# Kernel optimization log

Measured on AMD Instinct MI355X. Metric: run time of the kernel, lower is better.

## Reference

```python
import jax, jax.numpy as jnp
import numpy as np

N_NODES = 50000
N_EDGES = 800000


def setup_inputs() -> dict:
    key = jax.random.key(0)
    ks = jax.random.split(key, 12)
    x = jax.random.normal(ks[0], (N_NODES, 500), dtype=jnp.float32)
    edge_src = jax.random.randint(ks[1], (N_EDGES,), 0, N_NODES, dtype=jnp.int32)
    edge_dst = jax.random.randint(ks[2], (N_EDGES,), 0, N_NODES, dtype=jnp.int32)
    edge_vals = jax.random.uniform(ks[3], (N_EDGES,), dtype=jnp.float32) * 0.1
    def w(k, fan_in, fan_out):
        s = 1.0 / np.sqrt(fan_in)
        return jax.random.uniform(k, (fan_in, fan_out), dtype=jnp.float32, minval=-s, maxval=s)
    W1 = w(ks[4], 500, 128)
    b1 = jnp.zeros((128,), jnp.float32)
    W2 = w(ks[5], 128, 64)
    b2 = jnp.zeros((64,), jnp.float32)
    W3 = w(ks[6], 64, 16)
    b3 = jnp.zeros((16,), jnp.float32)
    We = w(ks[7], 64, 64)
    be = jnp.zeros((64,), jnp.float32)
    return {"x": x, "edge_vals": edge_vals, "W1": W1, "b1": b1, "W2": W2,
            "b2": b2, "W3": W3, "b3": b3, "We": We, "be": be,
            "edge_src": edge_src, "edge_dst": edge_dst}


def reference(x, edge_vals, W1, b1, W2, b2, W3, b3, We, be, edge_src, edge_dst):
    n = x.shape[0]

    def gcn_layer(h, W, b):
        # GraphConvolution: support = h @ W ; out = spmm(adj, support) + b
        support = h @ W                                   # [N, d_out]
        msg = support[edge_dst] * edge_vals[:, None]      # [E, d_out]
        agg = jax.ops.segment_sum(msg, edge_src, num_segments=n)
        return agg + b

    h = jax.nn.relu(gcn_layer(x, W1, b1))
    # dropout omitted (eval mode, training=False)
    h = jax.nn.relu(gcn_layer(h, W2, b2))
    out1 = jax.nn.log_softmax(gcn_layer(h, W3, b3), axis=1)
    out2 = h @ We + be
    return (out1, out2)
```

## Files before the change

kernel.cpp:

```cpp
#include <hip/hip_runtime.h>
#include <math.h>

#define N_NODES 50000
#define N_EDGES 800000

typedef __attribute__((ext_vector_type(8))) short bf16x8;
typedef __attribute__((ext_vector_type(4))) float f32x4;

__device__ inline unsigned short f2bf(float f) {
    unsigned u = __float_as_uint(f);
    unsigned r = (u + 0x7fffu + ((u >> 16) & 1u)) >> 16;
    return (unsigned short)r;
}

__global__ __launch_bounds__(256) void convert_weights_kernel(
    const float* __restrict__ W1, const float* __restrict__ W2,
    const float* __restrict__ We, const float* __restrict__ W3,
    unsigned short* __restrict__ W1bf, unsigned short* __restrict__ W2bf,
    unsigned short* __restrict__ Wcat)
{
    int t = blockIdx.x * 256 + threadIdx.x;
    if (t < 65536) {
        int n = t >> 9, k = t & 511;
        float v = (k < 500) ? W1[k * 128 + n] : 0.0f;
        W1bf[t] = f2bf(v);
    } else if (t < 65536 + 8192) {
        int t2 = t - 65536;
        int n = t2 >> 7, k = t2 & 127;
        W2bf[t2] = f2bf(W2[k * 64 + n]);
    } else if (t < 65536 + 8192 + 5120) {
        int t3 = t - 65536 - 8192;
        int n = t3 >> 6, k = t3 & 63;
        float v = (n < 64) ? We[k * 64 + n] : W3[k * 16 + (n - 64)];
        Wcat[t3] = f2bf(v);
    }
}

__global__ __launch_bounds__(256) void gemm1_mfma_kernel(
    const float* __restrict__ A,
    const unsigned short* __restrict__ Bt,
    unsigned short* __restrict__ C)
{
    const int wid  = (blockIdx.x * 256 + threadIdx.x) >> 6;
    const int lane = threadIdx.x & 63;
    const int r = lane & 15, q = lane >> 4;
    const int row0 = wid * 16;
    const int arow = row0 + r;
    const bool valid = arow < N_NODES;
    const float* ap = A + (size_t)arow * 500 + q * 8;

    const f32x4 zero = {0.0f, 0.0f, 0.0f, 0.0f};
    f32x4 acc[8];
#pragma unroll
    for (int j = 0; j < 8; ++j) acc[j] = zero;

#pragma unroll 4
    for (int s = 0; s < 16; ++s) {
        const int kb = s * 32 + q * 8;
        float4 a0 = make_float4(0.f, 0.f, 0.f, 0.f);
        float4 a1 = make_float4(0.f, 0.f, 0.f, 0.f);
        if (valid && kb < 500)
            a0 = *reinterpret_cast<const float4*>(ap + s * 32);
        if (valid && kb + 4 < 500)
            a1 = *reinterpret_cast<const float4*>(ap + s * 32 + 4);
        unsigned short h[8] = {f2bf(a0.x), f2bf(a0.y), f2bf(a0.z), f2bf(a0.w),
                               f2bf(a1.x), f2bf(a1.y), f2bf(a1.z), f2bf(a1.w)};
        bf16x8 af = *reinterpret_cast<bf16x8*>(h);
#pragma unroll
        for (int j = 0; j < 8; ++j) {
            bf16x8 bfr = *reinterpret_cast<const bf16x8*>(
                Bt + (size_t)(j * 16 + r) * 512 + s * 32 + q * 8);
            acc[j] = __builtin_amdgcn_mfma_f32_16x16x32_bf16(af, bfr, acc[j], 0, 0, 0);
        }
    }

#pragma unroll
    for (int reg = 0; reg < 4; ++reg) {
        int grow = row0 + q * 4 + reg;
        if (grow < N_NODES) {
#pragma unroll
            for (int j = 0; j < 8; ++j)
                C[(size_t)grow * 128 + j * 16 + r] = f2bf(acc[j][reg]);
        }
    }
}

__global__ __launch_bounds__(256) void gemm2_mfma_kernel(
    const unsigned short* __restrict__ A,
    const unsigned short* __restrict__ Bt,
    unsigned short* __restrict__ C)
{
    const int wid  = (blockIdx.x * 256 + threadIdx.x) >> 6;
    const int lane = threadIdx.x & 63;
    const int r = lane & 15, q = lane >> 4;
    const int row0 = wid * 16;
    const int arow = row0 + r;
    const bool valid = arow < N_NODES;
    const unsigned short* ap = A + (size_t)arow * 128 + q * 8;

    const f32x4 zero = {0.0f, 0.0f, 0.0f, 0.0f};
    f32x4 acc[4];
#pragma unroll
    for (int j = 0; j < 4; ++j) acc[j] = zero;

#pragma unroll
    for (int s = 0; s < 4; ++s) {
        bf16x8 af = {};
        if (valid) af = *reinterpret_cast<const bf16x8*>(ap + s * 32);
#pragma unroll
        for (int j = 0; j < 4; ++j) {
            bf16x8 bfr = *reinterpret_cast<const bf16x8*>(
                Bt + (size_t)(j * 16 + r) * 128 + s * 32 + q * 8);
            acc[j] = __builtin_amdgcn_mfma_f32_16x16x32_bf16(af, bfr, acc[j], 0, 0, 0);
        }
    }

#pragma unroll
    for (int reg = 0; reg < 4; ++reg) {
        int grow = row0 + q * 4 + reg;
        if (grow < N_NODES) {
#pragma unroll
            for (int j = 0; j < 4; ++j)
                C[(size_t)grow * 64 + j * 16 + r] = f2bf(acc[j][reg]);
        }
    }
}

__global__ __launch_bounds__(256) void gemm3_mfma_kernel(
    const unsigned short* __restrict__ A,
    const unsigned short* __restrict__ Bt,
    const float* __restrict__ be,
    float* __restrict__ out2,
    float* __restrict__ sup3)
{
    const int wid  = (blockIdx.x * 256 + threadIdx.x) >> 6;
    const int lane = threadIdx.x & 63;
    const int r = lane & 15, q = lane >> 4;
    const int row0 = wid * 16;
    const int arow = row0 + r;
    const bool valid = arow < N_NODES;
    const unsigned short* ap = A + (size_t)arow * 64 + q * 8;

    const f32x4 zero = {0.0f, 0.0f, 0.0f, 0.0f};
    f32x4 acc[5];
#pragma unroll
    for (int j = 0; j < 5; ++j) acc[j] = zero;

#pragma unroll
    for (int s = 0; s < 2; ++s) {
        bf16x8 af = {};
        if (valid) af = *reinterpret_cast<const bf16x8*>(ap + s * 32);
#pragma unroll
        for (int j = 0; j < 5; ++j) {
            bf16x8 bfr = *reinterpret_cast<const bf16x8*>(
                Bt + (size_t)(j * 16 + r) * 64 + s * 32 + q * 8);
            acc[j] = __builtin_amdgcn_mfma_f32_16x16x32_bf16(af, bfr, acc[j], 0, 0, 0);
        }
    }

    float bev[4];
#pragma unroll
    for (int j = 0; j < 4; ++j) bev[j] = be[j * 16 + r];

#pragma unroll
    for (int reg = 0; reg < 4; ++reg) {
        int grow = row0 + q * 4 + reg;
        if (grow < N_NODES) {
#pragma unroll
            for (int j = 0; j < 4; ++j)
                out2[(size_t)grow * 64 + j * 16 + r] = acc[j][reg] + bev[j];
            sup3[(size_t)grow * 16 + r] = acc[4][reg];
        }
    }
}

__global__ __launch_bounds__(256) void hist_kernel(
    const int* __restrict__ src, int* __restrict__ counts)
{
    int e = blockIdx.x * 256 + threadIdx.x;
    if (e < N_EDGES) atomicAdd(&counts[src[e]], 1);
}

__global__ __launch_bounds__(1024) void scan_kernel(
    const int* __restrict__ counts, int* __restrict__ row_ptr,
    int* __restrict__ cursor)
{
    constexpr int Q = N_NODES / 4;
    const int t = threadIdx.x;
    const int lane = t & 63, wave = t >> 6;
    __shared__ int wsum[16];
    __shared__ int carry_s;
    int carry = 0;
    const int4* c4 = reinterpret_cast<const int4*>(counts);
    int4* rp4 = reinterpret_cast<int4*>(row_ptr);
    int4* cu4 = reinterpret_cast<int4*>(cursor);

    for (int base = 0; base < Q; base += 1024) {
        const int g = base + t;
        int4 v = {0, 0, 0, 0};
        if (g < Q) v = c4[g];
        const int s = v.x + v.y + v.z + v.w;

        int incl = s;
#pragma unroll
        for (int off = 1; off < 64; off <<= 1) {
            int n = __shfl_up(incl, off, 64);
            if (lane >= off) incl += n;
        }
        if (lane == 63) wsum[wave] = incl;
        __syncthreads();
        if (t < 16) {
            int w = wsum[t];
            int inc = w;
#pragma unroll
            for (int off = 1; off < 16; off <<= 1) {
                int n = __shfl_up(inc, off, 64);
                if (t >= off) inc += n;
            }
            wsum[t] = inc - w;
            if (t == 15) carry_s = inc;
        }
        __syncthreads();
        if (g < Q) {
            int e0 = carry + wsum[wave] + (incl - s);
            int4 r;
            r.x = e0;
            r.y = r.x + v.x;
            r.z = r.y + v.y;
            r.w = r.z + v.z;
            rp4[g] = r;
            cu4[g] = r;
        }
        carry += carry_s;
        __syncthreads();
    }
    if (t == 0) row_ptr[N_NODES] = carry;
}

__global__ __launch_bounds__(256) void fill_kernel(
    const int* __restrict__ src, const int* __restrict__ dst,
    const float* __restrict__ vals, int* __restrict__ cursor,
    int2* __restrict__ pairs)
{
    int e = blockIdx.x * 256 + threadIdx.x;
    if (e >= N_EDGES) return;
    int pos = atomicAdd(&cursor[src[e]], 1);
    pairs[pos] = make_int2(dst[e], __float_as_int(vals[e]));
}

__global__ __launch_bounds__(256) void gather128_bf16_kernel(
    const unsigned short* __restrict__ support, const int2* __restrict__ pairs,
    const int* __restrict__ row_ptr, const float* __restrict__ b1,
    unsigned short* __restrict__ h1)
{
    const int node = blockIdx.x * 16 + (threadIdx.x >> 4);
    if (node >= N_NODES) return;
    const int lane = threadIdx.x & 15;
    int i = row_ptr[node];
    const int end = row_ptr[node + 1];

    float acc[8] = {};
    for (; i + 2 <= end; i += 2) {
        int2 p0 = pairs[i], p1 = pairs[i + 1];
        float v0 = __int_as_float(p0.y), v1 = __int_as_float(p1.y);
        uint4 r0 = *reinterpret_cast<const uint4*>(
            support + (size_t)p0.x * 128 + lane * 8);
        uint4 r1 = *reinterpret_cast<const uint4*>(
            support + (size_t)p1.x * 128 + lane * 8);
        unsigned w0[4] = {r0.x, r0.y, r0.z, r0.w};
        unsigned w1[4] = {r1.x, r1.y, r1.z, r1.w};
#pragma unroll
        for (int j = 0; j < 4; ++j) {
            acc[2 * j]     += __uint_as_float(w0[j] << 16) * v0;
            acc[2 * j + 1] += __uint_as_float(w0[j] & 0xffff0000u) * v0;
            acc[2 * j]     += __uint_as_float(w1[j] << 16) * v1;
            acc[2 * j + 1] += __uint_as_float(w1[j] & 0xffff0000u) * v1;
        }
    }
    if (i < end) {
        int2 p = pairs[i];
        float v = __int_as_float(p.y);
        uint4 r = *reinterpret_cast<const uint4*>(
            support + (size_t)p.x * 128 + lane * 8);
        unsigned w[4] = {r.x, r.y, r.z, r.w};
#pragma unroll
        for (int j = 0; j < 4; ++j) {
            acc[2 * j]     += __uint_as_float(w[j] << 16) * v;
            acc[2 * j + 1] += __uint_as_float(w[j] & 0xffff0000u) * v;
        }
    }
    const float4 ba = *reinterpret_cast<const float4*>(b1 + lane * 8);
    const float4 bb = *reinterpret_cast<const float4*>(b1 + lane * 8 + 4);
    float bias[8] = {ba.x, ba.y, ba.z, ba.w, bb.x, bb.y, bb.z, bb.w};
    unsigned short h[8];
#pragma unroll
    for (int j = 0; j < 8; ++j) {
        float v = acc[j] + bias[j];
        h[j] = f2bf(v > 0.0f ? v : 0.0f);
    }
    *reinterpret_cast<uint4*>(h1 + (size_t)node * 128 + lane * 8) =
        *reinterpret_cast<uint4*>(h);
}

__global__ __launch_bounds__(256) void gather64_bf16_kernel(
    const unsigned short* __restrict__ support, const int2* __restrict__ pairs,
    const int* __restrict__ row_ptr, const float* __restrict__ b2,
    unsigned short* __restrict__ h2)
{
    const int node = blockIdx.x * 32 + (threadIdx.x >> 3);
    if (node >= N_NODES) return;
    const int lane = threadIdx.x & 7;
    int i = row_ptr[node];
    const int end = row_ptr[node + 1];

    float acc[8] = {};
    for (; i + 2 <= end; i += 2) {
        int2 p0 = pairs[i], p1 = pairs[i + 1];
        float v0 = __int_as_float(p0.y), v1 = __int_as_float(p1.y);
        uint4 r0 = *reinterpret_cast<const uint4*>(
            support + (size_t)p0.x * 64 + lane * 8);
        uint4 r1 = *reinterpret_cast<const uint4*>(
            support + (size_t)p1.x * 64 + lane * 8);
        unsigned w0[4] = {r0.x, r0.y, r0.z, r0.w};
        unsigned w1[4] = {r1.x, r1.y, r1.z, r1.w};
#pragma unroll
        for (int j = 0; j < 4; ++j) {
            acc[2 * j]     += __uint_as_float(w0[j] << 16) * v0;
            acc[2 * j + 1] += __uint_as_float(w0[j] & 0xffff0000u) * v0;
            acc[2 * j]     += __uint_as_float(w1[j] << 16) * v1;
            acc[2 * j + 1] += __uint_as_float(w1[j] & 0xffff0000u) * v1;
        }
    }
    if (i < end) {
        int2 p = pairs[i];
        float v = __int_as_float(p.y);
        uint4 r = *reinterpret_cast<const uint4*>(
            support + (size_t)p.x * 64 + lane * 8);
        unsigned w[4] = {r.x, r.y, r.z, r.w};
#pragma unroll
        for (int j = 0; j < 4; ++j) {
            acc[2 * j]     += __uint_as_float(w[j] << 16) * v;
            acc[2 * j + 1] += __uint_as_float(w[j] & 0xffff0000u) * v;
        }
    }
    const float4 ba = *reinterpret_cast<const float4*>(b2 + lane * 8);
    const float4 bb = *reinterpret_cast<const float4*>(b2 + lane * 8 + 4);
    float bias[8] = {ba.x, ba.y, ba.z, ba.w, bb.x, bb.y, bb.z, bb.w};
    unsigned short h[8];
#pragma unroll
    for (int j = 0; j < 8; ++j) {
        float v = acc[j] + bias[j];
        h[j] = f2bf(v > 0.0f ? v : 0.0f);
    }
    *reinterpret_cast<uint4*>(h2 + (size_t)node * 64 + lane * 8) =
        *reinterpret_cast<uint4*>(h);
}

__global__ __launch_bounds__(256) void gather16_kernel(
    const float* __restrict__ support, const int2* __restrict__ pairs,
    const int* __restrict__ row_ptr, float* __restrict__ agg)
{
    const int node = blockIdx.x * 64 + (threadIdx.x >> 2);
    if (node >= N_NODES) return;
    const int lane = threadIdx.x & 3;
    int i = row_ptr[node];
    const int end = row_ptr[node + 1];

    float4 acc0 = {0, 0, 0, 0};
    float4 acc1 = {0, 0, 0, 0};

    for (; i + 2 <= end; i += 2) {
        int2 p0 = pairs[i];
        int2 p1 = pairs[i + 1];
        float v0 = __int_as_float(p0.y);
        float v1 = __int_as_float(p1.y);
        const float4 m0 = *reinterpret_cast<const float4*>(
            support + (size_t)p0.x * 16 + lane * 4);
        const float4 m1 = *reinterpret_cast<const float4*>(
            support + (size_t)p1.x * 16 + lane * 4);
        acc0.x += m0.x * v0; acc0.y += m0.y * v0;
        acc0.z += m0.z * v0; acc0.w += m0.w * v0;
        acc1.x += m1.x * v1; acc1.y += m1.y * v1;
        acc1.z += m1.z * v1; acc1.w += m1.w * v1;
    }
    if (i < end) {
        int2 p = pairs[i];
        float v = __int_as_float(p.y);
        const float4 m = *reinterpret_cast<const float4*>(
            support + (size_t)p.x * 16 + lane * 4);
        acc0.x += m.x * v; acc0.y += m.y * v;
        acc0.z += m.z * v; acc0.w += m.w * v;
    }
    acc0.x += acc1.x; acc0.y += acc1.y; acc0.z += acc1.z; acc0.w += acc1.w;
    *reinterpret_cast<float4*>(agg + (size_t)node * 16 + lane * 4) = acc0;
}

__global__ __launch_bounds__(256) void logsoftmax_kernel(
    const float* __restrict__ agg, const float* __restrict__ b3,
    float* __restrict__ out)
{
    int row = blockIdx.x * 256 + threadIdx.x;
    if (row >= N_NODES) return;
    float v[16];
    const float4* p = reinterpret_cast<const float4*>(agg + (size_t)row * 16);
#pragma unroll
    for (int i = 0; i < 4; ++i) {
        float4 q = p[i];
        v[i * 4 + 0] = q.x + b3[i * 4 + 0];
        v[i * 4 + 1] = q.y + b3[i * 4 + 1];
        v[i * 4 + 2] = q.z + b3[i * 4 + 2];
        v[i * 4 + 3] = q.w + b3[i * 4 + 3];
    }
    float mx = v[0];
#pragma unroll
    for (int i = 1; i < 16; ++i) mx = fmaxf(mx, v[i]);
    float s = 0.0f;
#pragma unroll
    for (int i = 0; i < 16; ++i) s += expf(v[i] - mx);
    float lse = mx + logf(s);
    float4* o = reinterpret_cast<float4*>(out + (size_t)row * 16);
#pragma unroll
    for (int i = 0; i < 4; ++i)
        o[i] = make_float4(v[i * 4 + 0] - lse, v[i * 4 + 1] - lse,
                           v[i * 4 + 2] - lse, v[i * 4 + 3] - lse);
}

extern "C" void kernel_launch(void* const* d_in, const int* in_sizes, int n_in,
                              void* d_out, int out_size, void* d_ws, size_t ws_size,
                              hipStream_t stream)
{
    const float* x         = (const float*)d_in[0];
    const float* edge_vals = (const float*)d_in[1];
    const float* W1 = (const float*)d_in[2];
    const float* b1 = (const float*)d_in[3];
    const float* W2 = (const float*)d_in[4];
    const float* b2 = (const float*)d_in[5];
    const float* W3 = (const float*)d_in[6];
    const float* b3 = (const float*)d_in[7];
    const float* We = (const float*)d_in[8];
    const float* be = (const float*)d_in[9];
    const int* esrc = (const int*)d_in[10];
    const int* edst = (const int*)d_in[11];

    float* out1 = (float*)d_out;
    float* out2 = (float*)d_out + (size_t)N_NODES * 16;

    char* ws = (char*)d_ws;
    float* bufA    = (float*)(ws);
    float* bufB    = (float*)(ws + 25600000);
    float* bufC    = (float*)(ws + 51200000);
    int*   counts  = (int*)  (ws + 54400000);
    int*   row_ptr = (int*)  (ws + 54600064);
    int*   cursor  = (int*)  (ws + 54800128);
    int2*  pairs   = (int2*) (ws + 55000192);

    unsigned short* W1bf = (unsigned short*)bufC;
    unsigned short* W2bf = (unsigned short*)((char*)bufC + 131072);
    unsigned short* Wcat = (unsigned short*)((char*)bufC + 147456);

    unsigned short* sup1bf = (unsigned short*)bufA;
    unsigned short* h1bf   = (unsigned short*)bufB;
    unsigned short* sup2bf = (unsigned short*)bufA;
    unsigned short* h2bf   = (unsigned short*)bufB;
    float*          sup3   = bufA;
    float*          agg3   = bufC;

    const int WB = (N_NODES / 16 + 3) / 4;
    const int EB = (N_EDGES + 255) / 256;

    convert_weights_kernel<<<308, 256, 0, stream>>>(W1, W2, We, W3, W1bf, W2bf, Wcat);
    hipMemsetAsync(counts, 0, (size_t)N_NODES * 4, stream);
    hist_kernel<<<EB, 256, 0, stream>>>(esrc, counts);
    scan_kernel<<<1, 1024, 0, stream>>>(counts, row_ptr, cursor);
    fill_kernel<<<EB, 256, 0, stream>>>(esrc, edst, edge_vals, cursor, pairs);

    gemm1_mfma_kernel<<<WB, 256, 0, stream>>>(x, W1bf, sup1bf);

    gather128_bf16_kernel<<<(N_NODES + 15) / 16, 256, 0, stream>>>(
        sup1bf, pairs, row_ptr, b1, h1bf);

    gemm2_mfma_kernel<<<WB, 256, 0, stream>>>(h1bf, W2bf, sup2bf);

    gather64_bf16_kernel<<<(N_NODES + 31) / 32, 256, 0, stream>>>(
        sup2bf, pairs, row_ptr, b2, h2bf);

    gemm3_mfma_kernel<<<WB, 256, 0, stream>>>(h2bf, Wcat, be, out2, sup3);

    gather16_kernel<<<(N_NODES + 63) / 64, 256, 0, stream>>>(
        sup3, pairs, row_ptr, agg3);

    logsoftmax_kernel<<<(N_NODES + 255) / 256, 256, 0, stream>>>(agg3, b3, out1);
}
```

Before: 417.1 us.

## Split GEMM1 output columns across two waves and software-prefetch next K-step

Each wave now computes a 16x64 output tile instead of 16x128, doubling the number of waves launched for the first GEMM. The loop also loads the A and B fragments for the next K-step before issuing the current MFMAs, so memory latency is hidden by explicit register double-buffering. The cost is that each row of x (fp32) is read and converted to bf16 twice, once per column half, which raises global traffic on the largest input. Prefetch also uses more registers.

```diff
diff --git a/kernel.cpp b/kernel.cpp
--- a/kernel.cpp
+++ b/kernel.cpp
@@ -41,47 +41,64 @@
     const unsigned short* __restrict__ Bt,
     unsigned short* __restrict__ C)
 {
-    const int wid  = (blockIdx.x * 256 + threadIdx.x) >> 6;
+    const int gwid = (blockIdx.x * 256 + threadIdx.x) >> 6;
     const int lane = threadIdx.x & 63;
     const int r = lane & 15, q = lane >> 4;
-    const int row0 = wid * 16;
+    const int row0 = (gwid >> 1) * 16;
+    const int col0 = (gwid & 1) * 64;
+    if (row0 >= N_NODES) return;
     const int arow = row0 + r;
-    const bool valid = arow < N_NODES;
     const float* ap = A + (size_t)arow * 500 + q * 8;
+    const unsigned short* bp = Bt + (size_t)(col0 + r) * 512 + q * 8;
 
     const f32x4 zero = {0.0f, 0.0f, 0.0f, 0.0f};
-    f32x4 acc[8];
-#pragma unroll
-    for (int j = 0; j < 8; ++j) acc[j] = zero;
-
-#pragma unroll 4
+    f32x4 acc[4];
+#pragma unroll
+    for (int j = 0; j < 4; ++j) acc[j] = zero;
+
+    float4 a0, a1;
+    bf16x8 bf[4];
+
+    auto loadA = [&](int s, float4& x0, float4& x1) {
+        const int kb = s * 32 + q * 8;
+        x0 = make_float4(0.f, 0.f, 0.f, 0.f);
+        x1 = make_float4(0.f, 0.f, 0.f, 0.f);
+        if (kb < 500)     x0 = *reinterpret_cast<const float4*>(ap + s * 32);
+        if (kb + 4 < 500) x1 = *reinterpret_cast<const float4*>(ap + s * 32 + 4);
+    };
+    auto loadB = [&](int s, bf16x8* d) {
+#pragma unroll
+        for (int j = 0; j < 4; ++j)
+            d[j] = *reinterpret_cast<const bf16x8*>(bp + (size_t)j * 16 * 512 + s * 32);
+    };
+
+    loadA(0, a0, a1);
+    loadB(0, bf);
+
     for (int s = 0; s < 16; ++s) {
-        const int kb = s * 32 + q * 8;
-        float4 a0 = make_float4(0.f, 0.f, 0.f, 0.f);
-        float4 a1 = make_float4(0.f, 0.f, 0.f, 0.f);
-        if (valid && kb < 500)
-            a0 = *reinterpret_cast<const float4*>(ap + s * 32);
-        if (valid && kb + 4 < 500)
-            a1 = *reinterpret_cast<const float4*>(ap + s * 32 + 4);
+        float4 na0, na1;
+        bf16x8 nb[4];
+        if (s < 15) {
+            loadA(s + 1, na0, na1);
+            loadB(s + 1, nb);
+        }
         unsigned short h[8] = {f2bf(a0.x), f2bf(a0.y), f2bf(a0.z), f2bf(a0.w),
                                f2bf(a1.x), f2bf(a1.y), f2bf(a1.z), f2bf(a1.w)};
         bf16x8 af = *reinterpret_cast<bf16x8*>(h);
 #pragma unroll
-        for (int j = 0; j < 8; ++j) {
-            bf16x8 bfr = *reinterpret_cast<const bf16x8*>(
-                Bt + (size_t)(j * 16 + r) * 512 + s * 32 + q * 8);
-            acc[j] = __builtin_amdgcn_mfma_f32_16x16x32_bf16(af, bfr, acc[j], 0, 0, 0);
-        }
+        for (int j = 0; j < 4; ++j)
+            acc[j] = __builtin_amdgcn_mfma_f32_16x16x32_bf16(af, bf[j], acc[j], 0, 0, 0);
+        a0 = na0; a1 = na1;
+#pragma unroll
+        for (int j = 0; j < 4; ++j) bf[j] = nb[j];
     }
 
 #pragma unroll
     for (int reg = 0; reg < 4; ++reg) {
-        int grow = row0 + q * 4 + reg;
-        if (grow < N_NODES) {
-#pragma unroll
-            for (int j = 0; j < 8; ++j)
-                C[(size_t)grow * 128 + j * 16 + r] = f2bf(acc[j][reg]);
-        }
+        const int grow = row0 + q * 4 + reg;
+#pragma unroll
+        for (int j = 0; j < 4; ++j)
+            C[(size_t)grow * 128 + col0 + j * 16 + r] = f2bf(acc[j][reg]);
     }
 }
 
@@ -466,6 +483,7 @@
     float*          agg3   = bufC;
 
     const int WB = (N_NODES / 16 + 3) / 4;
+    const int G1 = (2 * (N_NODES / 16) + 3) / 4;
     const int EB = (N_EDGES + 255) / 256;
 
     convert_weights_kernel<<<308, 256, 0, stream>>>(W1, W2, We, W3, W1bf, W2bf, Wcat);
@@ -474,7 +492,7 @@
     scan_kernel<<<1, 1024, 0, stream>>>(counts, row_ptr, cursor);
     fill_kernel<<<EB, 256, 0, stream>>>(esrc, edst, edge_vals, cursor, pairs);
 
-    gemm1_mfma_kernel<<<WB, 256, 0, stream>>>(x, W1bf, sup1bf);
+    gemm1_mfma_kernel<<<G1, 256, 0, stream>>>(x, W1bf, sup1bf);
 
     gather128_bf16_kernel<<<(N_NODES + 15) / 16, 256, 0, stream>>>(
         sup1bf, pairs, row_ptr, b1, h1bf);
```

After: 427.1 us. +2.4%, slower.

## Stage W1 fragments in LDS and make gemm1 a persistent column-split kernel

Applied to the files above, without the earlier changes.

The first-layer weights are pre-permuted into MFMA fragment order so that each block can copy its 64-column half into 64KB of LDS. Each wave then reads B fragments from LDS instead of global memory. gemm1 becomes a persistent 512-block kernel that loops over 16-row tiles. Blocks are split by column half, so every row of x is read by two blocks, which relies on L2 hits. Boundary predicates are replaced by clamped loads, since the weight fragments are zero-padded past K=500, and fp32-to-bf16 packing now uses the HIP intrinsics.

```diff
diff --git a/kernel.cpp b/kernel.cpp
--- a/kernel.cpp
+++ b/kernel.cpp
@@ -1,4 +1,5 @@
 #include <hip/hip_runtime.h>
+#include <hip/hip_bf16.h>
 #include <math.h>
 
 #define N_NODES 50000
@@ -13,17 +14,34 @@
     return (unsigned short)r;
 }
 
+__device__ inline bf16x8 pack8(float4 a0, float4 a1) {
+    union { __hip_bfloat162 h2[4]; bf16x8 v; } u;
+    u.h2[0] = __float22bfloat162_rn(make_float2(a0.x, a0.y));
+    u.h2[1] = __float22bfloat162_rn(make_float2(a0.z, a0.w));
+    u.h2[2] = __float22bfloat162_rn(make_float2(a1.x, a1.y));
+    u.h2[3] = __float22bfloat162_rn(make_float2(a1.z, a1.w));
+    return u.v;
+}
+
 __global__ __launch_bounds__(256) void convert_weights_kernel(
     const float* __restrict__ W1, const float* __restrict__ W2,
     const float* __restrict__ We, const float* __restrict__ W3,
-    unsigned short* __restrict__ W1bf, unsigned short* __restrict__ W2bf,
+    unsigned short* __restrict__ W1frag, unsigned short* __restrict__ W2bf,
     unsigned short* __restrict__ Wcat)
 {
     int t = blockIdx.x * 256 + threadIdx.x;
     if (t < 65536) {
-        int n = t >> 9, k = t & 511;
+        int h = t >> 15;
+        int r1 = t & 32767;
+        int j = r1 >> 13;
+        int r2 = r1 & 8191;
+        int s = r2 >> 9;
+        int r3 = r2 & 511;
+        int lane = r3 >> 3, jj = r3 & 7;
+        int k = s * 32 + (lane >> 4) * 8 + jj;
+        int n = h * 64 + j * 16 + (lane & 15);
         float v = (k < 500) ? W1[k * 128 + n] : 0.0f;
-        W1bf[t] = f2bf(v);
+        W1frag[t] = f2bf(v);
     } else if (t < 65536 + 8192) {
         int t2 = t - 65536;
         int n = t2 >> 7, k = t2 & 127;
@@ -36,51 +54,60 @@
     }
 }
 
-__global__ __launch_bounds__(256) void gemm1_mfma_kernel(
+__global__ __launch_bounds__(256, 2) void gemm1_mfma_kernel(
     const float* __restrict__ A,
-    const unsigned short* __restrict__ Bt,
+    const unsigned short* __restrict__ W1frag,
     unsigned short* __restrict__ C)
 {
-    const int wid  = (blockIdx.x * 256 + threadIdx.x) >> 6;
-    const int lane = threadIdx.x & 63;
+    __shared__ __align__(16) unsigned short Bs[32768];
+
+    const int t = threadIdx.x;
+    const int h  = blockIdx.x & 1;
+    const int br = blockIdx.x >> 1;
+    const int lane = t & 63;
+    const int wave = t >> 6;
     const int r = lane & 15, q = lane >> 4;
-    const int row0 = wid * 16;
-    const int arow = row0 + r;
-    const bool valid = arow < N_NODES;
-    const float* ap = A + (size_t)arow * 500 + q * 8;
-
-    const f32x4 zero = {0.0f, 0.0f, 0.0f, 0.0f};
-    f32x4 acc[8];
-#pragma unroll
-    for (int j = 0; j < 8; ++j) acc[j] = zero;
+
+    {
+        const uint4* src = reinterpret_cast<const uint4*>(W1frag + h * 32768);
+        uint4* dst = reinterpret_cast<uint4*>(Bs);
+#pragma unroll
+        for (int i = 0; i < 16; ++i)
+            dst[t + i * 256] = src[t + i * 256];
+    }
+    __syncthreads();
+
+    const int col0 = h * 64;
+
+    for (int c = br * 4 + wave; c < 3125; c += 1024) {
+        const float* ap = A + (size_t)(c * 16 + r) * 500;
+
+        f32x4 acc[4];
+#pragma unroll
+        for (int j = 0; j < 4; ++j) acc[j] = {0.f, 0.f, 0.f, 0.f};
 
 #pragma unroll 4
-    for (int s = 0; s < 16; ++s) {
-        const int kb = s * 32 + q * 8;
-        float4 a0 = make_float4(0.f, 0.f, 0.f, 0.f);
-        float4 a1 = make_float4(0.f, 0.f, 0.f, 0.f);
-        if (valid && kb < 500)
-            a0 = *reinterpret_cast<const float4*>(ap + s * 32);
-        if (valid && kb + 4 < 500)
-            a1 = *reinterpret_cast<const float4*>(ap + s * 32 + 4);
-        unsigned short h[8] = {f2bf(a0.x), f2bf(a0.y), f2bf(a0.z), f2bf(a0.w),
-                               f2bf(a1.x), f2bf(a1.y), f2bf(a1.z), f2bf(a1.w)};
-        bf16x8 af = *reinterpret_cast<bf16x8*>(h);
-#pragma unroll
-        for (int j = 0; j < 8; ++j) {
-            bf16x8 bfr = *reinterpret_cast<const bf16x8*>(
-                Bt + (size_t)(j * 16 + r) * 512 + s * 32 + q * 8);
-            acc[j] = __builtin_amdgcn_mfma_f32_16x16x32_bf16(af, bfr, acc[j], 0, 0, 0);
-        }
-    }
-
-#pragma unroll
-    for (int reg = 0; reg < 4; ++reg) {
-        int grow = row0 + q * 4 + reg;
-        if (grow < N_NODES) {
-#pragma unroll
-            for (int j = 0; j < 8; ++j)
-                C[(size_t)grow * 128 + j * 16 + r] = f2bf(acc[j][reg]);
+        for (int s = 0; s < 16; ++s) {
+            const int kb = s * 32 + q * 8;
+            const int k0 = kb < 496 ? kb : 496;
+            const int k1 = (kb + 4) < 496 ? (kb + 4) : 496;
+            float4 a0 = *reinterpret_cast<const float4*>(ap + k0);
+            float4 a1 = *reinterpret_cast<const float4*>(ap + k1);
+            bf16x8 af = pack8(a0, a1);
+#pragma unroll
+            for (int j = 0; j < 4; ++j) {
+                bf16x8 b = *reinterpret_cast<const bf16x8*>(
+                    &Bs[(size_t)((j * 16 + s) * 64 + lane) * 8]);
+                acc[j] = __builtin_amdgcn_mfma_f32_16x16x32_bf16(af, b, acc[j], 0, 0, 0);
+            }
+        }
+
+#pragma unroll
+        for (int reg = 0; reg < 4; ++reg) {
+            const int grow = c * 16 + q * 4 + reg;
+#pragma unroll
+            for (int j = 0; j < 4; ++j)
+                C[(size_t)grow * 128 + col0 + j * 16 + r] = f2bf(acc[j][reg]);
         }
     }
 }
@@ -454,7 +481,7 @@
     int*   cursor  = (int*)  (ws + 54800128);
     int2*  pairs   = (int2*) (ws + 55000192);
 
-    unsigned short* W1bf = (unsigned short*)bufC;
+    unsigned short* W1frag = (unsigned short*)bufC;
     unsigned short* W2bf = (unsigned short*)((char*)bufC + 131072);
     unsigned short* Wcat = (unsigned short*)((char*)bufC + 147456);
 
@@ -468,13 +495,13 @@
     const int WB = (N_NODES / 16 + 3) / 4;
     const int EB = (N_EDGES + 255) / 256;
 
-    convert_weights_kernel<<<308, 256, 0, stream>>>(W1, W2, We, W3, W1bf, W2bf, Wcat);
+    convert_weights_kernel<<<308, 256, 0, stream>>>(W1, W2, We, W3, W1frag, W2bf, Wcat);
     hipMemsetAsync(counts, 0, (size_t)N_NODES * 4, stream);
     hist_kernel<<<EB, 256, 0, stream>>>(esrc, counts);
     scan_kernel<<<1, 1024, 0, stream>>>(counts, row_ptr, cursor);
     fill_kernel<<<EB, 256, 0, stream>>>(esrc, edst, edge_vals, cursor, pairs);
 
-    gemm1_mfma_kernel<<<WB, 256, 0, stream>>>(x, W1bf, sup1bf);
+    gemm1_mfma_kernel<<<512, 256, 0, stream>>>(x, W1frag, sup1bf);
 
     gather128_bf16_kernel<<<(N_NODES + 15) / 16, 256, 0, stream>>>(
         sup1bf, pairs, row_ptr, b1, h1bf);
```

Measured after the change: 371.1 us. -11.0%, faster.
